# Kernel tuning notes

Hardware: AMD Instinct MI355X
Metric: run time of the kernel (lower is better)

## Reference

```python
import jax, jax.numpy as jnp
import numpy as np

N, E, IN_F, HID, MSG, OUT, P = 512, 2048, 64, 256, 128, 16, 4
MAX_STEPS = 10 * N  # message cap from the torch while-loop: messages < num_nodes*10


def _lin_init(k, o, i):
    kw, kb = jax.random.split(k)
    s = 1.0 / np.sqrt(i)
    return (jax.random.uniform(kw, (o, i), jnp.float32, -s, s),
            jax.random.uniform(kb, (o,), jnp.float32, -s, s))


def setup_inputs() -> dict:
    key = jax.random.key(0)
    ks = jax.random.split(key, 12)
    xa = jax.random.normal(ks[0], (N, IN_F), jnp.float32)
    first_message = jax.random.normal(ks[1], (N, MSG), jnp.float32)
    edge_index = jax.random.randint(ks[2], (2, E), 0, N, jnp.int32)
    starts = jax.random.randint(ks[3], (N,), 0, 2, jnp.int32)
    enc_W, enc_b = _lin_init(ks[4], HID, IN_F)
    s = 1.0 / np.sqrt(HID)
    W_ih = jax.random.uniform(ks[5], (4 * HID, MSG), jnp.float32, -s, s)
    W_hh = jax.random.uniform(ks[6], (4 * HID, HID), jnp.float32, -s, s)
    b_ih = jax.random.uniform(ks[7], (4 * HID,), jnp.float32, -s, s)
    b_hh = jax.random.uniform(ks[8], (4 * HID,), jnp.float32, -s, s)
    nm_W, nm_b = _lin_init(ks[9], MSG, HID + MSG)
    dec_W = jax.random.uniform(ks[10], (P, OUT, HID), jnp.float32, -s, s)
    dec_b = jax.random.uniform(ks[11], (P, OUT), jnp.float32, -s, s)
    return dict(xa=xa, first_message=first_message, edge_index=edge_index, starts=starts,
                enc_W=enc_W, enc_b=enc_b, W_ih=W_ih, W_hh=W_hh, b_ih=b_ih, b_hh=b_hh,
                nm_W=nm_W, nm_b=nm_b, dec_W=dec_W, dec_b=dec_b)


def _prep_graph(edge_index, starts):
    # Static (non-differentiable) graph preprocessing, mirrors GwACLSTM.neighbors:
    # undirected neighbor *sets*, iterated in sorted order.
    src, dst = np.asarray(edge_index)
    nbr = [set() for _ in range(N)]
    for s, d in zip(src.tolist(), dst.tolist()):
        nbr[s].add(d)
        nbr[d].add(s)
    degs = np.array([len(s) for s in nbr], np.int32)
    maxd = max(1, int(degs.max()))
    nbrs = np.zeros((N, maxd), np.int32)
    for i, s in enumerate(nbr):
        nbrs[i, :len(s)] = sorted(s)
    start_nodes = np.nonzero(np.asarray(starts))[0].astype(np.int32)
    return jnp.asarray(nbrs), jnp.asarray(degs), jnp.asarray(start_nodes), maxd


def _forward(xa, first_message, enc_W, enc_b, W_ih, W_hh, b_ih, b_hh,
             nm_W, nm_b, dec_W, dec_b, nbrs, degs, start_nodes, maxd):
    S0 = int(start_nodes.shape[0])
    cap = S0 + MAX_STEPS * maxd  # queue can never exceed this
    hid = xa @ enc_W.T + enc_b   # per-node initial hidden state = encoder(xa)
    cell = jnp.zeros_like(hid)
    q_nodes = jnp.zeros((cap,), jnp.int32).at[:S0].set(start_nodes)
    q_msgs = jnp.zeros((cap, MSG), xa.dtype)
    if S0 > 0:
        q_msgs = q_msgs.at[:S0, :].set(first_message[start_nodes])

    def step(carry, i):
        q_nodes, q_msgs, hid, cell, t = carry
        node, msg = q_nodes[i], q_msgs[i]
        h_prev, c_prev = hid[node], cell[node]
        # torch.nn.LSTMCell: gates ordered i, f, g, o
        gates = msg @ W_ih.T + b_ih + h_prev @ W_hh.T + b_hh
        gi, gf, gg, go = jnp.split(gates, 4)
        c_new = jax.nn.sigmoid(gf) * c_prev + jax.nn.sigmoid(gi) * jnp.tanh(gg)
        h_new = jax.nn.sigmoid(go) * jnp.tanh(c_new)
        new_msg = jnp.concatenate([h_new, msg]) @ nm_W.T + nm_b
        active = i < t  # queue nonempty
        hid = hid.at[node].set(jnp.where(active, h_new, h_prev))
        cell = cell.at[node].set(jnp.where(active, c_new, c_prev))
        # enqueue new_msg for every neighbor; slots beyond degs[node] are
        # overwritten by later enqueues (tail only advances by degs[node])
        q_nodes = jax.lax.dynamic_update_slice(q_nodes, nbrs[node], (t,))
        q_msgs = jax.lax.dynamic_update_slice(
            q_msgs, jnp.broadcast_to(new_msg, (maxd, MSG)), (t, 0))
        t = jnp.where(active, t + degs[node], t)
        return (q_nodes, q_msgs, hid, cell, t), None

    init = (q_nodes, q_msgs, hid, cell, jnp.int32(S0))
    (_, _, hid, _, _), _ = jax.lax.scan(step, init, jnp.arange(MAX_STEPS, dtype=jnp.int32))
    # graph_class=False: per-node predictions from each decoder head
    logits = jnp.einsum('nh,poh->pno', hid, dec_W) + dec_b[:, None, :]
    return jax.nn.log_softmax(logits, axis=-1)  # [P, N, OUT]


def reference(xa, first_message, edge_index, starts, enc_W, enc_b, W_ih, W_hh,
              b_ih, b_hh, nm_W, nm_b, dec_W, dec_b):
    nbrs, degs, start_nodes, maxd = _prep_graph(edge_index, starts)
    return _forward(xa, first_message, enc_W, enc_b, W_ih, W_hh, b_ih, b_hh,
                    nm_W, nm_b, dec_W, dec_b, nbrs, degs, start_nodes, maxd)
```

## Files before the change

kernel.cpp:

```cpp
#include <hip/hip_runtime.h>
#include <math.h>

#define NN 512
#define EE 2048
#define IN_F 64
#define HID 256
#define MSGD 128
#define OUTC 16
#define MAX_STEPS 5120

#define NWGA 256
#define MAXD 64
#define NCLUS 32
#define WPC 8
#define KSLOT 16

typedef _Float16 h2v __attribute__((ext_vector_type(2)));
typedef _Float16 f16x8 __attribute__((ext_vector_type(8)));
typedef float f32x4 __attribute__((ext_vector_type(4)));

static __device__ __forceinline__ float fdot2u(unsigned int w, unsigned int a, float c) {
    return __builtin_amdgcn_fdot2(__builtin_bit_cast(h2v, w),
                                  __builtin_bit_cast(h2v, a), c, false);
}
static __device__ __forceinline__ unsigned int pkh(float a, float b) {
    h2v h; h.x = (_Float16)a; h.y = (_Float16)b;
    return __builtin_bit_cast(unsigned int, h);
}

__device__ int   g_nbrs64[NN][MAXD];
__device__ int   g_degs[NN];
__device__ int4  g_sched[MAX_STEPS];
__device__ int   g_mready[MAX_STEPS];
__device__ int   g_S0, g_T, g_P;
__device__ int   g_alist[NWGA][MAX_STEPS];
__device__ int   g_acnt[NWGA];
__device__ int   g_noff[NN + 1];
__device__ int   g_nlist[MAX_STEPS];
__device__ int   g_border[NN];
__device__ int   g_nB;
__device__ int   g_tflag[NCLUS][WPC];
__device__ float g_qmsgs[MAX_STEPS][MSGD];
__device__ uint4 g_qmsgP4[MAX_STEPS][16];
__device__ uint4 g_hpk4[2][NN][32];
__device__ float g_hid[NN][HID];
__device__ float g_cell[NN][HID];
__device__ uint4 g_WTph[112 * 512];
__device__ uint4 g_WBm[WPC * 8 * 12 * 64];
__device__ unsigned int g_nmTph[192 * 128];
__device__ float g_bias[1024];

__device__ __forceinline__ float sigm(float x) { return 1.0f / (1.0f + expf(-x)); }
__device__ __forceinline__ float gw(const float* W_ih, const float* W_hh, int row, int c) {
    return (c < MSGD) ? W_ih[row * MSGD + c] : W_hh[row * HID + (c - MSGD)];
}

__global__ __launch_bounds__(256) void k_setup(const float* __restrict__ xa,
                                               const float* __restrict__ enc_W,
                                               const float* __restrict__ enc_b,
                                               const float* __restrict__ W_ih,
                                               const float* __restrict__ W_hh,
                                               const float* __restrict__ b_ih,
                                               const float* __restrict__ b_hh,
                                               const float* __restrict__ nm_W,
                                               const int* __restrict__ edge_index) {
    const int b = blockIdx.x, tid = threadIdx.x;
    if (b < 512) {
        const int gid = b * 256 + tid;
        const int n = gid >> 8, ccol = gid & 255;
        const float* x = xa + n * IN_F;
        const float* w = enc_W + ccol * IN_F;
        float acc = enc_b[ccol];
#pragma unroll 8
        for (int j = 0; j < IN_F; ++j) acc += x[j] * w[j];
        g_hid[n][ccol] = acc;
        g_cell[n][ccol] = 0.0f;
    } else if (b < 1024) {
        const int r = b - 512;
        for (int q = tid; q < 96; q += 256) {
            uint4 v;
            v.x = pkh(gw(W_ih, W_hh, 2 * r, 4 * q),     gw(W_ih, W_hh, 2 * r, 4 * q + 1));
            v.y = pkh(gw(W_ih, W_hh, 2 * r + 1, 4 * q), gw(W_ih, W_hh, 2 * r + 1, 4 * q + 1));
            v.z = pkh(gw(W_ih, W_hh, 2 * r, 4 * q + 2), gw(W_ih, W_hh, 2 * r, 4 * q + 3));
            v.w = pkh(gw(W_ih, W_hh, 2 * r + 1, 4 * q + 2), gw(W_ih, W_hh, 2 * r + 1, 4 * q + 3));
            g_WTph[q * 512 + r] = v;
        }
        if (r < 192 && tid < 128)
            g_nmTph[r * 128 + tid] = pkh(nm_W[tid * 384 + 2 * r], nm_W[tid * 384 + 2 * r + 1]);
        if (r == 0)
            for (int g = tid; g < 1024; g += 256) g_bias[g] = b_ih[g] + b_hh[g];
    } else if (b < 1216) {
        const int b4 = (b - 1024) * 4 + (tid >> 6);
        const int lane = tid & 63;
        const int j = b4 / 96, rem = b4 - j * 96;
        const int w = rem / 12, kt = rem - w * 12;
        const int rl = 16 * w + (lane & 15);
        const int R = (rl >> 5) * 256 + (j << 5) + (rl & 31);
        const int kb = kt * 32 + (lane >> 4) * 8;
        unsigned int d[4];
#pragma unroll
        for (int q = 0; q < 4; ++q)
            d[q] = pkh(gw(W_ih, W_hh, R, kb + 2 * q), gw(W_ih, W_hh, R, kb + 2 * q + 1));
        uint4 v; v.x = d[0]; v.y = d[1]; v.z = d[2]; v.w = d[3];
        g_WBm[b4 * 64 + lane] = v;
    } else {
        __shared__ unsigned int bits[16];
        const int v = b - 1216;
        if (tid < 16) bits[tid] = 0u;
        __syncthreads();
        for (int e = tid; e < EE; e += 256) {
            const int s = edge_index[e], d = edge_index[EE + e];
            if (s == v) atomicOr(&bits[d >> 5], 1u << (d & 31));
            if (d == v) atomicOr(&bits[s >> 5], 1u << (s & 31));
        }
        __syncthreads();
        if (tid == 0) {
            int cnt = 0;
            for (int w = 0; w < 16; ++w) {
                unsigned int bb = bits[w];
                while (bb) {
                    const int j = __ffs(bb) - 1;
                    bb &= bb - 1u;
                    if (cnt < MAXD) g_nbrs64[v][cnt++] = w * 32 + j;
                }
            }
            g_degs[v] = cnt;
        }
    }
}

__global__ __launch_bounds__(1024) void k_sched(const int* __restrict__ starts) {
    __shared__ int s_nx[MAX_STEPS];
    __shared__ int s_ny[MAX_STEPS];
    __shared__ int scanbuf[2][1024];
    __shared__ int s_deg[NN];
    __shared__ int s_off[NN + 1];
    __shared__ int s_csr[4160];
    __shared__ int s_nodes[NN];
    __shared__ int s_cnt[NN];
    __shared__ int s_misc[4];
    __shared__ int s_hist[64];
    const int tid = threadIdx.x;

    const int stt = (tid < NN && starts[tid] != 0) ? 1 : 0;
    const int dg0 = (tid < NN) ? g_degs[tid] : 0;
    if (tid < NN) s_deg[tid] = dg0;
    for (int i = tid; i < MAX_STEPS; i += 1024) s_ny[i] = 0x7fffffff;

    scanbuf[0][tid] = dg0;
    __syncthreads();
    int src = 0;
    for (int off = 1; off < 1024; off <<= 1) {
        int v = scanbuf[src][tid];
        if (tid >= off) v += scanbuf[src][tid - off];
        scanbuf[src ^ 1][tid] = v;
        src ^= 1;
        __syncthreads();
    }
    if (tid <= NN) s_off[tid] = scanbuf[src][tid] - ((tid < NN) ? dg0 : 0);
    __syncthreads();

    scanbuf[0][tid] = stt;
    __syncthreads();
    src = 0;
    for (int off = 1; off < 1024; off <<= 1) {
        int v = scanbuf[src][tid];
        if (tid >= off) v += scanbuf[src][tid - off];
        scanbuf[src ^ 1][tid] = v;
        src ^= 1;
        __syncthreads();
    }
    if (stt) s_nodes[scanbuf[src][tid] - 1] = tid;
    const int S0tot = scanbuf[src][1023];
    __syncthreads();

    if (tid < NN) {
        const int o = s_off[tid], dg = s_deg[tid];
        for (int e = 0; e < dg; ++e) s_csr[o + e] = g_nbrs64[tid][e];
    }
    const int S0 = (S0tot < MAX_STEPS) ? S0tot : MAX_STEPS;
    int known = S0;
    for (int i = tid; i < known; i += 1024) s_nx[i] = s_nodes[i];
    __syncthreads();

    for (int round = 0; round < 8 && known > 0; ++round) {
        const int C = (known + 1023) >> 10;
        const int base = tid * C;
        int lsum = 0;
        for (int j = 0; j < C; ++j) {
            int i = base + j;
            if (i < known) lsum += s_deg[s_nx[i]];
        }
        scanbuf[0][tid] = lsum;
        __syncthreads();
        src = 0;
        for (int off = 1; off < 1024; off <<= 1) {
            int v = scanbuf[src][tid];
            if (tid >= off) v += scanbuf[src][tid - off];
            scanbuf[src ^ 1][tid] = v;
            src ^= 1;
            __syncthreads();
        }
        const int excl = (tid == 0) ? 0 : scanbuf[src][tid - 1];
        const int total = scanbuf[src][1023];
        int t = S0 + excl;
        for (int j = 0; j < C; ++j) {
            int i = base + j;
            if (i < known) {
                const int nd = s_nx[i];
                const int dg = s_deg[nd], o = s_off[nd];
                s_ny[i] = t;
                for (int e = 0; e < dg; ++e) {
                    const int pos = t + e;
                    if (pos >= known && pos < MAX_STEPS) s_nx[pos] = s_csr[o + e];
                }
                t += dg;
            }
        }
        __syncthreads();
        int newknown = S0 + total;
        if (newknown > MAX_STEPS) newknown = MAX_STEPS;
        if (newknown == known) break;
        known = newknown;
    }
    __syncthreads();
    const int kn = known;
    if (tid == 0) s_misc[1] = kn;
    __syncthreads();
    for (int i = tid; i < kn; i += 1024)
        if (s_ny[i] <= i) atomicMin(&s_misc[1], i);
    __syncthreads();
    const int istar = s_misc[1];
    if (tid == 0) s_misc[2] = istar;
    __syncthreads();
    for (int i = tid; i < istar; i += 1024)
        if (s_ny[i] >= istar) atomicMin(&s_misc[2], i);
    __syncthreads();
    const int P = s_misc[2];

    for (int i = tid; i < MAX_STEPS; i += 1024) {
        int4 sc;
        if (i < kn) { sc.x = s_nx[i]; sc.y = s_ny[i]; sc.z = s_deg[sc.x]; }
        else { sc.x = 0; sc.y = 0x7fffffff; sc.z = 0; }
        sc.w = 0;
        g_sched[i] = sc;
    }
    if (tid == 0) { g_S0 = S0; g_T = istar; g_P = P; }

    if (tid < NN) s_cnt[tid] = 0;
    __syncthreads();
    for (int i = P + tid; i < istar; i += 1024) atomicAdd(&s_cnt[s_nx[i]], 1);
    __syncthreads();
    const int cnt0 = (tid < NN) ? s_cnt[tid] : 0;
    scanbuf[0][tid] = cnt0;
    __syncthreads();
    src = 0;
    for (int off = 1; off < 1024; off <<= 1) {
        int v = scanbuf[src][tid];
        if (tid >= off) v += scanbuf[src][tid - off];
        scanbuf[src ^ 1][tid] = v;
        src ^= 1;
        __syncthreads();
    }
    if (tid <= NN) g_noff[tid] = scanbuf[src][tid] - ((tid < NN) ? cnt0 : 0);

    if (tid < 64) s_hist[tid] = 0;
    __syncthreads();
    if (tid < NN && cnt0 > 0) atomicAdd(&s_hist[(cnt0 < 63) ? cnt0 : 63], 1);
    __syncthreads();
    if (tid == 0) {
        int acc = 0;
        for (int b = 63; b >= 1; --b) { const int t = s_hist[b]; s_hist[b] = acc; acc += t; }
        g_nB = acc;
    }
    __syncthreads();
    if (tid < NN && cnt0 > 0) {
        const int p = atomicAdd(&s_hist[(cnt0 < 63) ? cnt0 : 63], 1);
        g_border[p] = tid;
    }
    if (tid < NCLUS * WPC) g_tflag[tid >> 3][tid & 7] = -1;

    for (int i = tid; i < MAX_STEPS; i += 1024) g_mready[i] = (i < S0) ? 1 : 0;
}

__global__ __launch_bounds__(256) void k_lists2(const float* __restrict__ first_message) {
    __shared__ int sWOff[4];
    __shared__ int sBase;
    const int b = blockIdx.x, tid = threadIdx.x;
    const int lane = tid & 63, wv = tid >> 6;
    if (b < NN) {
        const int v = b;
        const int lo = g_P, hi = g_T;
        if (tid == 0) sBase = g_noff[v];
        __syncthreads();
        for (int st = lo; st < hi; st += 256) {
            const int i = st + tid;
            const bool m = (i < hi) && (g_sched[i].x == v);
            const unsigned long long bal = __ballot(m);
            const int rank = __popcll(bal & ((1ull << lane) - 1ull));
            if (lane == 0) sWOff[wv] = __popcll(bal);
            __syncthreads();
            if (tid == 0) {
                int acc = sBase;
                for (int w = 0; w < 4; ++w) { const int t = sWOff[w]; sWOff[w] = acc; acc += t; }
                sBase = acc;
            }
            __syncthreads();
            if (m) g_nlist[sWOff[wv] + rank] = i;
            __syncthreads();
        }
    } else if (b < NN + NWGA) {
        const int w0 = b - NN;
        const int hi = g_P;
        if (tid == 0) sBase = 0;
        __syncthreads();
        for (int st = 0; st < hi; st += 256) {
            const int i = st + tid;
            const bool m = (i < hi) && ((g_sched[i].x & (NWGA - 1)) == w0);
            const unsigned long long bal = __ballot(m);
            const int rank = __popcll(bal & ((1ull << lane) - 1ull));
            if (lane == 0) sWOff[wv] = __popcll(bal);
            __syncthreads();
            if (tid == 0) {
                int acc = sBase;
                for (int w = 0; w < 4; ++w) { const int t = sWOff[w]; sWOff[w] = acc; acc += t; }
                sBase = acc;
            }
            __syncthreads();
            if (m) g_alist[w0][sWOff[wv] + rank] = i;
            __syncthreads();
        }
        if (tid == 0) g_acnt[w0] = sBase;
    } else {
        const int i = (b - NN - NWGA) * 2 + (tid >> 7);
        const int col = tid & 127;
        if (i < g_S0) g_qmsgs[i][col] = first_message[g_sched[i].x * MSGD + col];
    }
}

__global__ __launch_bounds__(512, 1) void k_phaseA(const float* __restrict__ nm_b) {
    __shared__ float sAct[MSGD];
    __shared__ float sNH[2][HID], sNC[2][HID];
    __shared__ float sGates[1024];
    __shared__ float sPart[4 * MSGD];
    __shared__ unsigned int sActP[192];
    __shared__ unsigned int sActN[192];
    const int tid = threadIdx.x, wg = blockIdx.x;
    const int cntA = g_acnt[wg];
    if (cntA == 0) return;
    const int S0 = g_S0, T = g_T;
    const float vb0 = g_bias[2 * tid], vb1 = g_bias[2 * tid + 1];
    const uint4* wp = g_WTph + tid;

    for (int idx = tid; idx < 2 * HID; idx += 512) {
        int sl = idx >> 8, u = idx & 255, v = wg + (sl << 8);
        sNH[sl][u] = g_hid[v][u];
        sNC[sl][u] = g_cell[v][u];
    }
    __syncthreads();

    for (int k = 0; k < cntA; ++k) {
        const int s = g_alist[wg][k];
        const int4 sc = g_sched[s];
        const int node = sc.x, y = sc.y, deg = sc.z, sl = node >> 8;
        if (s >= S0) {
            if (tid == 0) {
                while (__hip_atomic_load(&g_mready[s], __ATOMIC_RELAXED,
                                         __HIP_MEMORY_SCOPE_AGENT) == 0)
                    __builtin_amdgcn_s_sleep(2);
            }
            __syncthreads();
            __builtin_amdgcn_fence(__ATOMIC_ACQUIRE, "workgroup");
        }
        if (tid < 64) {
            float a0, a1;
            if (s < S0) { a0 = g_qmsgs[s][2 * tid]; a1 = g_qmsgs[s][2 * tid + 1]; }
            else {
                a0 = __hip_atomic_load(&g_qmsgs[s][2 * tid],     __ATOMIC_RELAXED,
                                       __HIP_MEMORY_SCOPE_AGENT);
                a1 = __hip_atomic_load(&g_qmsgs[s][2 * tid + 1], __ATOMIC_RELAXED,
                                       __HIP_MEMORY_SCOPE_AGENT);
            }
            sAct[2 * tid] = a0; sAct[2 * tid + 1] = a1;
            sActP[tid] = pkh(a0, a1);
        } else if (tid < 192) {
            const int j = tid - 64;
            sActP[tid] = pkh(sNH[sl][2 * j], sNH[sl][2 * j + 1]);
        }
        __syncthreads();
        {
            float acc0 = vb0, acc1 = vb1;
            uint4 wA[8], wB[8];
#pragma unroll
            for (int j = 0; j < 8; ++j) wA[j] = wp[j * 512];
#pragma unroll
            for (int j = 0; j < 8; ++j) wB[j] = wp[(8 + j) * 512];
#pragma unroll 1
            for (int qb = 0; qb < 96; qb += 16) {
#pragma unroll
                for (int j = 0; j < 8; ++j) {
                    const int q = qb + j;
                    const unsigned int a01 = sActP[2 * q], a23 = sActP[2 * q + 1];
                    acc0 = fdot2u(wA[j].x, a01, acc0); acc1 = fdot2u(wA[j].y, a01, acc1);
                    acc0 = fdot2u(wA[j].z, a23, acc0); acc1 = fdot2u(wA[j].w, a23, acc1);
                }
#pragma unroll
                for (int j = 0; j < 8; ++j) wA[j] = wp[(qb + 16 + j) * 512];
#pragma unroll
                for (int j = 0; j < 8; ++j) {
                    const int q = qb + 8 + j;
                    const unsigned int a01 = sActP[2 * q], a23 = sActP[2 * q + 1];
                    acc0 = fdot2u(wB[j].x, a01, acc0); acc1 = fdot2u(wB[j].y, a01, acc1);
                    acc0 = fdot2u(wB[j].z, a23, acc0); acc1 = fdot2u(wB[j].w, a23, acc1);
                }
#pragma unroll
                for (int j = 0; j < 8; ++j) wB[j] = wp[(qb + 24 + j) * 512];
            }
            ((float2*)sGates)[tid] = make_float2(acc0, acc1);
        }
        __syncthreads();
        if (tid < HID) {
            const int u = tid;
            const float gi = sGates[u], gf = sGates[256 + u];
            const float gg = sGates[512 + u], go = sGates[768 + u];
            const float cp = sNC[sl][u];
            const float cn = sigm(gf) * cp + sigm(gi) * tanhf(gg);
            const float hn = sigm(go) * tanhf(cn);
            sNC[sl][u] = cn;
            sNH[sl][u] = hn;
        }
        __syncthreads();
        if (tid < 128) sActN[tid] = pkh(sNH[sl][2 * tid], sNH[sl][2 * tid + 1]);
        else if (tid < 192) {
            const int j = tid - 128;
            sActN[tid] = pkh(sAct[2 * j], sAct[2 * j + 1]);
        }
        __syncthreads();
        {
            const int o = tid & (MSGD - 1), cq = tid >> 7;
            float p = 0.0f;
#pragma unroll 8
            for (int j = 0; j < 48; ++j) {
                const int cp = 48 * cq + j;
                p = fdot2u(g_nmTph[cp * 128 + o], sActN[cp], p);
            }
            sPart[cq * MSGD + o] = p;
        }
        __syncthreads();
        const int lim = (y + deg <= T) ? deg : (T - y);
        if (tid < MSGD) {
            const float m = nm_b[tid] + sPart[tid] + sPart[MSGD + tid]
                          + sPart[2 * MSGD + tid] + sPart[3 * MSGD + tid];
            const float mN = __shfl_down(m, 1);
            for (int e = 0; e < lim; ++e)
                __hip_atomic_store(&g_qmsgs[y + e][tid], m, __ATOMIC_RELAXED,
                                   __HIP_MEMORY_SCOPE_AGENT);
            if ((tid & 1) == 0) {
                const unsigned int pm = pkh(m, mN);
                unsigned int* pd = (unsigned int*)g_qmsgP4;
                for (int e = 0; e < lim; ++e) pd[(y + e) * 64 + (tid >> 1)] = pm;
            }
        }
        __syncthreads();
        if (tid < lim)
            __hip_atomic_store(&g_mready[y + tid], 1, __ATOMIC_RELAXED,
                               __HIP_MEMORY_SCOPE_AGENT);
    }
    __syncthreads();
    for (int idx = tid; idx < 2 * HID; idx += 512) {
        int sl = idx >> 8, u = idx & 255, v = wg + (sl << 8);
        g_hid[v][u]  = sNH[sl][u];
        g_cell[v][u] = sNC[sl][u];
    }
}

__global__ __launch_bounds__(512, 1) void k_phaseB() {
    __shared__ uint4 sB[12 * 64];
    __shared__ float sG[128][17];
    __shared__ float sC[KSLOT][32];
    __shared__ int sNode[KSLOT], sLen[KSLOT], sOff[KSLOT], sStep[KSLOT];
    __shared__ int sMaxLen;
    const int tid = threadIdx.x, wg = blockIdx.x;
    const int c = wg >> 3, j = wg & 7;
    const int wv = tid >> 6, lane = tid & 63;
    const int nB = g_nB;

    if (tid < KSLOT) {
        const int ci = tid * NCLUS + c;
        if (ci < nB) {
            const int v = g_border[ci];
            sNode[tid] = v;
            sOff[tid]  = g_noff[v];
            sLen[tid]  = g_noff[v + 1] - g_noff[v];
        } else { sNode[tid] = -1; sLen[tid] = 0; sOff[tid] = 0; }
    }
    if (tid == 0) sMaxLen = 0;
    __syncthreads();
    if (tid < KSLOT) atomicMax(&sMaxLen, sLen[tid]);
    __syncthreads();
    const int maxlen = sMaxLen;
    if (maxlen == 0) return;

    {
        uint4 z; z.x = z.y = z.z = z.w = 0u;
        for (int i = tid; i < 12 * 64; i += 512) sB[i] = z;
    }
    f16x8 afr[12];
    {
        const f16x8* src = (const f16x8*)g_WBm + ((j * 8 + wv) * 12) * 64 + lane;
#pragma unroll
        for (int kt = 0; kt < 12; ++kt) afr[kt] = src[kt * 64];
    }
    f32x4 bias;
#pragma unroll
    for (int r = 0; r < 4; ++r) {
        const int rl = 16 * wv + (lane >> 4) * 4 + r;
        bias[r] = g_bias[(rl >> 5) * 256 + (j << 5) + (rl & 31)];
    }
    {
        const int k = tid >> 5, u = tid & 31;
        if (sNode[k] >= 0) sC[k][u] = g_cell[sNode[k]][(j << 5) + u];
    }
    for (int idx = tid; idx < KSLOT * 16; idx += 512) {
        const int k = idx >> 4, d = idx & 15;
        if (sNode[k] >= 0) {
            const float h0 = g_hid[sNode[k]][(j << 5) + 2 * d];
            const float h1 = g_hid[sNode[k]][(j << 5) + 2 * d + 1];
            __hip_atomic_store((unsigned int*)g_hpk4[1][sNode[k]] + (j << 4) + d,
                               pkh(h0, h1), __ATOMIC_RELAXED, __HIP_MEMORY_SCOPE_AGENT);
        }
    }
    __syncthreads();
    if (tid == 0)
        __hip_atomic_store(&g_tflag[c][j], 0, __ATOMIC_RELAXED, __HIP_MEMORY_SCOPE_AGENT);

    for (int tick = 0; tick < maxlen; ++tick) {
        if (tid < KSLOT) sStep[tid] = (tick < sLen[tid]) ? g_nlist[sOff[tid] + tick] : -1;
        __syncthreads();
        for (int idx = tid; idx < 4 * 64; idx += 512) {
            const int l = idx & 63, kt = idx >> 6;
            const int n = l & 15, s = sStep[n];
            if (s >= 0) sB[kt * 64 + l] = g_qmsgP4[s][kt * 4 + (l >> 4)];
        }
        if (tid < WPC) {
            while (__hip_atomic_load(&g_tflag[c][tid], __ATOMIC_RELAXED,
                                     __HIP_MEMORY_SCOPE_AGENT) < tick)
                __builtin_amdgcn_s_sleep(1);
        }
        __syncthreads();
        const int pb = (tick + 1) & 1;
        for (int idx = tid; idx < 8 * 64; idx += 512) {
            const int l = idx & 63, kt = 4 + (idx >> 6);
            const int n = l & 15, s = sStep[n];
            if (s >= 0) {
                const int g = kt * 4 + (l >> 4) - 16;
                const unsigned long long* hp =
                    (const unsigned long long*)g_hpk4[pb][sNode[n]];
                const unsigned long long lo = __hip_atomic_load(
                    hp + g * 2, __ATOMIC_RELAXED, __HIP_MEMORY_SCOPE_AGENT);
                const unsigned long long hi = __hip_atomic_load(
                    hp + g * 2 + 1, __ATOMIC_RELAXED, __HIP_MEMORY_SCOPE_AGENT);
                uint4 val;
                val.x = (unsigned int)lo; val.y = (unsigned int)(lo >> 32);
                val.z = (unsigned int)hi; val.w = (unsigned int)(hi >> 32);
                sB[kt * 64 + l] = val;
            }
        }
        __syncthreads();
        {
            f32x4 acc = bias;
#pragma unroll
            for (int kt = 0; kt < 12; ++kt) {
                const f16x8 bfr = ((const f16x8*)sB)[kt * 64 + lane];
                acc = __builtin_amdgcn_mfma_f32_16x16x32_f16(afr[kt], bfr, acc, 0, 0, 0);
            }
            const int n = lane & 15, rbase = 16 * wv + (lane >> 4) * 4;
#pragma unroll
            for (int r = 0; r < 4; ++r) sG[rbase + r][n] = acc[r];
        }
        __syncthreads();
        {
            const int k = tid >> 5, u = tid & 31;
            const int v = sNode[k];
            const bool act = (sStep[k] >= 0);
            float hn = 0.0f;
            if (act) {
                const float gi = sG[u][k],      gf = sG[32 + u][k];
                const float gg = sG[64 + u][k], go = sG[96 + u][k];
                const float cn = sigm(gf) * sC[k][u] + sigm(gi) * tanhf(gg);
                sC[k][u] = cn;
                hn = sigm(go) * tanhf(cn);
            }
            const float hn1 = __shfl_down(hn, 1);
            if (act) {
                if ((u & 1) == 0) {
                    unsigned int* dst = (unsigned int*)g_hpk4[tick & 1][v];
                    __hip_atomic_store(&dst[(j << 4) + (u >> 1)], pkh(hn, hn1),
                                       __ATOMIC_RELAXED, __HIP_MEMORY_SCOPE_AGENT);
                }
                if (tick == sLen[k] - 1) g_hid[v][(j << 5) + u] = hn;
            }
        }
        __syncthreads();
        if (tid == 0)
            __hip_atomic_store(&g_tflag[c][j], tick + 1, __ATOMIC_RELAXED,
                               __HIP_MEMORY_SCOPE_AGENT);
    }
}

__global__ __launch_bounds__(256) void k_decode(const float* __restrict__ dec_W,
                                                const float* __restrict__ dec_b,
                                                float* __restrict__ out) {
    const int gtid = blockIdx.x * 256 + threadIdx.x;
    const int row = gtid >> 4, lane = gtid & 15;
    const int p = row >> 9, n = row & (NN - 1);
    const float* dw = dec_W + (p * OUTC + lane) * HID;
    float acc = dec_b[p * OUTC + lane];
#pragma unroll 8
    for (int j = 0; j < HID; j += 4) {
        const float4 hv = *(const float4*)&g_hid[n][j];
        const float4 wv = *(const float4*)(dw + j);
        acc += hv.x * wv.x + hv.y * wv.y + hv.z * wv.z + hv.w * wv.w;
    }
    float mx = acc;
    mx = fmaxf(mx, __shfl_xor(mx, 1));
    mx = fmaxf(mx, __shfl_xor(mx, 2));
    mx = fmaxf(mx, __shfl_xor(mx, 4));
    mx = fmaxf(mx, __shfl_xor(mx, 8));
    float s = expf(acc - mx);
    s += __shfl_xor(s, 1);
    s += __shfl_xor(s, 2);
    s += __shfl_xor(s, 4);
    s += __shfl_xor(s, 8);
    out[row * OUTC + lane] = acc - mx - logf(s);
}

extern "C" void kernel_launch(void* const* d_in, const int* in_sizes, int n_in,
                              void* d_out, int out_size, void* d_ws, size_t ws_size,
                              hipStream_t stream) {
    (void)in_sizes; (void)n_in; (void)out_size; (void)d_ws; (void)ws_size;
    const float* xa   = (const float*)d_in[0];
    const float* fm   = (const float*)d_in[1];
    const int*   ei   = (const int*)d_in[2];
    const int*   st   = (const int*)d_in[3];
    const float* encW = (const float*)d_in[4];
    const float* encb = (const float*)d_in[5];
    const float* Wih  = (const float*)d_in[6];
    const float* Whh  = (const float*)d_in[7];
    const float* bih  = (const float*)d_in[8];
    const float* bhh  = (const float*)d_in[9];
    const float* nmW  = (const float*)d_in[10];
    const float* nmb  = (const float*)d_in[11];
    const float* decW = (const float*)d_in[12];
    const float* decb = (const float*)d_in[13];
    float* out = (float*)d_out;

    hipLaunchKernelGGL(k_setup,  dim3(1728),            dim3(256),  0, stream,
                       xa, encW, encb, Wih, Whh, bih, bhh, nmW, ei);
    hipLaunchKernelGGL(k_sched,  dim3(1),               dim3(1024), 0, stream, st);
    hipLaunchKernelGGL(k_lists2, dim3(NN + NWGA + 256), dim3(256),  0, stream, fm);
    hipLaunchKernelGGL(k_phaseA, dim3(NWGA),            dim3(512),  0, stream, nmb);
    hipLaunchKernelGGL(k_phaseB, dim3(NCLUS * WPC),     dim3(512),  0, stream);
    hipLaunchKernelGGL(k_decode, dim3(128),             dim3(256),  0, stream, decW, decb, out);
}
```

Measured before the change: 216.7 us.

## Compute hidden-state gate contribution before waiting on incoming message

Splits the per-step LSTM gate matvec so the W_hh·h part (the hidden-state half of the packed activation) is computed before spinning on the message-ready flag. Only the message part (W_ih·msg) is computed after the wait. This moves most of the dot-product work off the critical dependency chain between producer and consumer workgroups. It adds an extra barrier per step and keeps more accumulator and weight registers live across the wait.

```diff
diff --git a/kernel.cpp b/kernel.cpp
--- a/kernel.cpp
+++ b/kernel.cpp
@@ -363,6 +363,44 @@
         const int s = g_alist[wg][k];
         const int4 sc = g_sched[s];
         const int node = sc.x, y = sc.y, deg = sc.z, sl = node >> 8;
+
+        if (tid >= 64 && tid < 192) {
+            const int jx = tid - 64;
+            sActP[tid] = pkh(sNH[sl][2 * jx], sNH[sl][2 * jx + 1]);
+        }
+        __syncthreads();
+
+        float acc0 = vb0, acc1 = vb1;
+        {
+            const uint4* wph = wp + 32 * 512;
+            uint4 wA[8], wB[8];
+#pragma unroll
+            for (int j = 0; j < 8; ++j) wA[j] = wph[j * 512];
+#pragma unroll
+            for (int j = 0; j < 8; ++j) wB[j] = wph[(8 + j) * 512];
+#pragma unroll 1
+            for (int qb = 0; qb < 64; qb += 16) {
+#pragma unroll
+                for (int j = 0; j < 8; ++j) {
+                    const int q = 32 + qb + j;
+                    const unsigned int a01 = sActP[2 * q], a23 = sActP[2 * q + 1];
+                    acc0 = fdot2u(wA[j].x, a01, acc0); acc1 = fdot2u(wA[j].y, a01, acc1);
+                    acc0 = fdot2u(wA[j].z, a23, acc0); acc1 = fdot2u(wA[j].w, a23, acc1);
+                }
+#pragma unroll
+                for (int j = 0; j < 8; ++j) wA[j] = wph[(qb + 16 + j) * 512];
+#pragma unroll
+                for (int j = 0; j < 8; ++j) {
+                    const int q = 32 + qb + 8 + j;
+                    const unsigned int a01 = sActP[2 * q], a23 = sActP[2 * q + 1];
+                    acc0 = fdot2u(wB[j].x, a01, acc0); acc1 = fdot2u(wB[j].y, a01, acc1);
+                    acc0 = fdot2u(wB[j].z, a23, acc0); acc1 = fdot2u(wB[j].w, a23, acc1);
+                }
+#pragma unroll
+                for (int j = 0; j < 8; ++j) wB[j] = wph[(qb + 24 + j) * 512];
+            }
+        }
+
         if (s >= S0) {
             if (tid == 0) {
                 while (__hip_atomic_load(&g_mready[s], __ATOMIC_RELAXED,
@@ -383,20 +421,16 @@
             }
             sAct[2 * tid] = a0; sAct[2 * tid + 1] = a1;
             sActP[tid] = pkh(a0, a1);
-        } else if (tid < 192) {
-            const int j = tid - 64;
-            sActP[tid] = pkh(sNH[sl][2 * j], sNH[sl][2 * j + 1]);
         }
         __syncthreads();
         {
-            float acc0 = vb0, acc1 = vb1;
             uint4 wA[8], wB[8];
 #pragma unroll
             for (int j = 0; j < 8; ++j) wA[j] = wp[j * 512];
 #pragma unroll
             for (int j = 0; j < 8; ++j) wB[j] = wp[(8 + j) * 512];
 #pragma unroll 1
-            for (int qb = 0; qb < 96; qb += 16) {
+            for (int qb = 0; qb < 32; qb += 16) {
 #pragma unroll
                 for (int j = 0; j < 8; ++j) {
                     const int q = qb + j;
```

New measurement: 313.4 us. 1.45x slower.
